# Performance work log

Measured on AMD Instinct MI355X. Metric: run time of the kernel, lower is better.

The kernel has to match this reference:

```python
import jax, jax.numpy as jnp
import numpy as np

NUM_CODES = 1296
D_DIM = 64


def setup_inputs() -> dict:
    key = jax.random.key(0)
    k1, k2 = jax.random.split(key)
    inputs = jax.random.normal(k1, (32, 64, 64, D_DIM), dtype=jnp.float32)
    # lecun_normal init: stddev = 1/sqrt(fan_in) with fan_in = d
    embeddings = jax.random.normal(k2, (NUM_CODES, D_DIM), dtype=jnp.float32) / np.sqrt(D_DIM)
    return {"inputs": inputs, "embeddings": embeddings}


def reference(inputs, embeddings):
    x1 = jnp.sum(inputs ** 2, axis=-1, keepdims=True)          # [b,m,n,1]
    x2 = jnp.sum(embeddings ** 2, axis=-1)                      # [k]
    x3 = jnp.einsum('bmnd,kd->bmnk', inputs, embeddings)        # [b,m,n,k]
    D = x1 + x2 - 2.0 * x3
    codes = jnp.argmin(D, axis=-1).astype(jnp.int32)            # [b,m,n]
    code_vecs = embeddings[codes]                               # [b,m,n,d]
    return codes, code_vecs
```

## Files before the change

### kernel.cpp

```cpp
#include <hip/hip_runtime.h>

#define NUM_CODES 1296
#define PAD_CODES 1344
#define DDIM 64
#define NUM_Q 131072
#define THREADS 256
#define QPW 32
#define QPB 128
#define MARGIN 0.25f
#define CAP 512
#define CHUNK 96
#define NSTEP 14
#define TPC 6

typedef __attribute__((ext_vector_type(8))) short bf16x8;
typedef __attribute__((ext_vector_type(4))) float f32x4;

__device__ __forceinline__ ushort f2bf(float f) {
    unsigned u = __float_as_uint(f);
    return (ushort)((u + 0x7fffu + ((u >> 16) & 1u)) >> 16);
}

__global__ __launch_bounds__(64) void vq_prep(const float* __restrict__ emb,
                                              float* __restrict__ enorm,
                                              ushort* __restrict__ eh) {
    int k = blockIdx.x * 64 + threadIdx.x;
    if (k >= PAD_CODES) return;
    int ks = k < NUM_CODES ? k : NUM_CODES - 1;
    const float* e = emb + (size_t)ks * DDIM;
    float f[DDIM];
#pragma unroll
    for (int i = 0; i < 16; ++i) {
        float4 v = *(const float4*)(e + 4 * i);
        f[4*i] = v.x; f[4*i+1] = v.y; f[4*i+2] = v.z; f[4*i+3] = v.w;
    }
    {
#pragma clang fp contract(off)
        float r8[8];
#pragma unroll
        for (int j = 0; j < 8; ++j) { float t = f[j] * f[j]; r8[j] = t; }
#pragma unroll
        for (int i = 1; i < 8; ++i) {
#pragma unroll
            for (int j = 0; j < 8; ++j) { float t = f[i*8+j] * f[i*8+j]; r8[j] += t; }
        }
        enorm[k] = ((r8[0]+r8[1])+(r8[2]+r8[3])) + ((r8[4]+r8[5])+(r8[6]+r8[7]));
    }
    ushort h[DDIM];
#pragma unroll
    for (int d = 0; d < DDIM; ++d) h[d] = f2bf(f[d]);
    uint* dh = (uint*)(eh + (size_t)k * DDIM);
#pragma unroll
    for (int s = 0; s < 8; ++s) {
        int ds = s ^ (k & 7);
#pragma unroll
        for (int j = 0; j < 4; ++j)
            dh[ds*4 + j] = (uint)h[s*8 + 2*j] | ((uint)h[s*8 + 2*j + 1] << 16);
    }
}

__global__ __launch_bounds__(256) void vq_xnorm(const float* __restrict__ x,
                                                float* __restrict__ xnorm) {
    int q = blockIdx.x * 256 + threadIdx.x;
    const float* r = x + (size_t)q * DDIM;
    float f[DDIM];
#pragma unroll
    for (int i = 0; i < 16; ++i) {
        float4 v = *(const float4*)(r + 4 * i);
        f[4*i] = v.x; f[4*i+1] = v.y; f[4*i+2] = v.z; f[4*i+3] = v.w;
    }
    {
#pragma clang fp contract(off)
        float r8[8];
#pragma unroll
        for (int j = 0; j < 8; ++j) { float t = f[j] * f[j]; r8[j] = t; }
#pragma unroll
        for (int i = 1; i < 8; ++i) {
#pragma unroll
            for (int j = 0; j < 8; ++j) { float t = f[i*8+j] * f[i*8+j]; r8[j] += t; }
        }
        xnorm[q] = ((r8[0]+r8[1])+(r8[2]+r8[3])) + ((r8[4]+r8[5])+(r8[6]+r8[7]));
    }
}

__global__ __launch_bounds__(THREADS) void vq_main(
        const float* __restrict__ x, const float* __restrict__ emb,
        const float* __restrict__ enorm_g, const float* __restrict__ xnorm,
        const ushort* __restrict__ eh, float* __restrict__ out) {
    __shared__ ushort sbuf[2][CHUNK * DDIM];
    __shared__ unsigned wq[4][CAP];
    __shared__ unsigned wcnt[4];
    __shared__ unsigned long long best64[4][QPW];

    const int tid  = threadIdx.x;
    const int lane = tid & 63;
    const int w    = tid >> 6;
    const int cl   = lane & 15;
    const int g    = lane >> 4;
    const long qw  = (long)blockIdx.x * QPB + w * QPW;

    if (lane < QPW) best64[w][lane] = ~0ULL;
    if (lane == 0) wcnt[w] = 0;

    bf16x8 a00, a01, a10, a11;
    {
        const float* xp0 = x + (qw + cl) * DDIM + g * 8;
        const float* xp1 = xp0 + 16 * DDIM;
#pragma unroll
        for (int j = 0; j < 8; ++j) {
            a00[j] = (short)f2bf(xp0[j]);
            a01[j] = (short)f2bf(xp0[j + 32]);
            a10[j] = (short)f2bf(xp1[j]);
            a11[j] = (short)f2bf(xp1[j + 32]);
        }
    }

    float rmin0[4], rmin1[4];
#pragma unroll
    for (int r = 0; r < 4; ++r) { rmin0[r] = __builtin_inff(); rmin1[r] = __builtin_inff(); }

    const int slot0 = (g     ^ (cl & 7)) * 8;
    const int slot1 = ((g+4) ^ (cl & 7)) * 8;

    {
        const float4* src = (const float4*)eh;
        float4 s0 = src[tid], s1 = src[256 + tid], s2 = src[512 + tid];
        *(float4*)&sbuf[0][(size_t)tid * 8]         = s0;
        *(float4*)&sbuf[0][(size_t)(256 + tid) * 8] = s1;
        *(float4*)&sbuf[0][(size_t)(512 + tid) * 8] = s2;
    }
    __syncthreads();
    int cur = 0;
    for (int s = 0; s < NSTEP; ++s) {
        float4 n0, n1, n2;
        const bool more = (s + 1 < NSTEP);
        if (more) {
            const float4* src = (const float4*)(eh + (size_t)(s + 1) * CHUNK * DDIM);
            n0 = src[tid]; n1 = src[256 + tid]; n2 = src[512 + tid];
        }
        const int cb = s * CHUNK;
        float en[TPC];
#pragma unroll
        for (int t = 0; t < TPC; ++t) en[t] = enorm_g[cb + t * 16 + cl];
#pragma unroll
        for (int t = 0; t < TPC; ++t) {
            const ushort* bp = &sbuf[cur][(size_t)(t * 16 + cl) * DDIM];
            bf16x8 b0 = *(const bf16x8*)(bp + slot0);
            bf16x8 b1 = *(const bf16x8*)(bp + slot1);
            f32x4 c00 = {0,0,0,0}, c01 = {0,0,0,0}, c10 = {0,0,0,0}, c11 = {0,0,0,0};
            c00 = __builtin_amdgcn_mfma_f32_16x16x32_bf16(a00, b0, c00, 0, 0, 0);
            c10 = __builtin_amdgcn_mfma_f32_16x16x32_bf16(a10, b0, c10, 0, 0, 0);
            c01 = __builtin_amdgcn_mfma_f32_16x16x32_bf16(a01, b1, c01, 0, 0, 0);
            c11 = __builtin_amdgcn_mfma_f32_16x16x32_bf16(a11, b1, c11, 0, 0, 0);
#pragma unroll
            for (int r = 0; r < 4; ++r) {
                rmin0[r] = fminf(rmin0[r], fmaf(-2.f, c00[r] + c01[r], en[t]));
                rmin1[r] = fminf(rmin1[r], fmaf(-2.f, c10[r] + c11[r], en[t]));
            }
        }
        if (more) {
            *(float4*)&sbuf[cur ^ 1][(size_t)tid * 8]         = n0;
            *(float4*)&sbuf[cur ^ 1][(size_t)(256 + tid) * 8] = n1;
            *(float4*)&sbuf[cur ^ 1][(size_t)(512 + tid) * 8] = n2;
        }
        __syncthreads();
        cur ^= 1;
    }

#pragma unroll
    for (int m = 1; m < 16; m <<= 1) {
#pragma unroll
        for (int r = 0; r < 4; ++r) {
            rmin0[r] = fminf(rmin0[r], __shfl_xor(rmin0[r], m, 64));
            rmin1[r] = fminf(rmin1[r], __shfl_xor(rmin1[r], m, 64));
        }
    }
#pragma unroll
    for (int r = 0; r < 4; ++r) { rmin0[r] += MARGIN; rmin1[r] += MARGIN; }

    {
        const float4* src = (const float4*)eh;
        float4 s0 = src[tid], s1 = src[256 + tid], s2 = src[512 + tid];
        *(float4*)&sbuf[cur][(size_t)tid * 8]         = s0;
        *(float4*)&sbuf[cur][(size_t)(256 + tid) * 8] = s1;
        *(float4*)&sbuf[cur][(size_t)(512 + tid) * 8] = s2;
    }
    __syncthreads();
    for (int s = 0; s < NSTEP; ++s) {
        float4 n0, n1, n2;
        const bool more = (s + 1 < NSTEP);
        if (more) {
            const float4* src = (const float4*)(eh + (size_t)(s + 1) * CHUNK * DDIM);
            n0 = src[tid]; n1 = src[256 + tid]; n2 = src[512 + tid];
        }
        const int cb = s * CHUNK;
        float en[TPC];
#pragma unroll
        for (int t = 0; t < TPC; ++t) en[t] = enorm_g[cb + t * 16 + cl];
#pragma unroll
        for (int t = 0; t < TPC; ++t) {
            const ushort* bp = &sbuf[cur][(size_t)(t * 16 + cl) * DDIM];
            bf16x8 b0 = *(const bf16x8*)(bp + slot0);
            bf16x8 b1 = *(const bf16x8*)(bp + slot1);
            f32x4 c00 = {0,0,0,0}, c01 = {0,0,0,0}, c10 = {0,0,0,0}, c11 = {0,0,0,0};
            c00 = __builtin_amdgcn_mfma_f32_16x16x32_bf16(a00, b0, c00, 0, 0, 0);
            c10 = __builtin_amdgcn_mfma_f32_16x16x32_bf16(a10, b0, c10, 0, 0, 0);
            c01 = __builtin_amdgcn_mfma_f32_16x16x32_bf16(a01, b1, c01, 0, 0, 0);
            c11 = __builtin_amdgcn_mfma_f32_16x16x32_bf16(a11, b1, c11, 0, 0, 0);
            const int c_ = cb + t * 16 + cl;
#pragma unroll
            for (int r = 0; r < 4; ++r) {
                float s0_ = fmaf(-2.f, c00[r] + c01[r], en[t]);
                float s1_ = fmaf(-2.f, c10[r] + c11[r], en[t]);
                if (c_ < NUM_CODES && s0_ <= rmin0[r]) {
                    unsigned i_ = atomicAdd(&wcnt[w], 1u);
                    if (i_ < CAP) wq[w][i_] = ((unsigned)(g*4 + r) << 11) | (unsigned)c_;
                }
                if (c_ < NUM_CODES && s1_ <= rmin1[r]) {
                    unsigned i_ = atomicAdd(&wcnt[w], 1u);
                    if (i_ < CAP) wq[w][i_] = ((unsigned)(16 + g*4 + r) << 11) | (unsigned)c_;
                }
            }
        }
        if (more) {
            *(float4*)&sbuf[cur ^ 1][(size_t)tid * 8]         = n0;
            *(float4*)&sbuf[cur ^ 1][(size_t)(256 + tid) * 8] = n1;
            *(float4*)&sbuf[cur ^ 1][(size_t)(512 + tid) * 8] = n2;
        }
        __syncthreads();
        cur ^= 1;
    }

    unsigned cnt = wcnt[w]; if (cnt > CAP) cnt = CAP;
    for (unsigned i = lane; i < cnt; i += 64) {
        unsigned p = wq[w][i];
        int ql = (int)(p >> 11); int c = (int)(p & 0x7FFu);
        long gq = qw + ql;
        const float* xr = x + gq * DDIM;
        const float* er = emb + (size_t)c * DDIM;
        float dot = 0.f;
#pragma unroll
        for (int p4 = 0; p4 < 16; ++p4) {
            float4 xv = *(const float4*)(xr + 4 * p4);
            float4 ev = *(const float4*)(er + 4 * p4);
            dot = fmaf(xv.x, ev.x, dot); dot = fmaf(xv.y, ev.y, dot);
            dot = fmaf(xv.z, ev.z, dot); dot = fmaf(xv.w, ev.w, dot);
        }
        float dist = (xnorm[gq] + enorm_g[c]) - 2.f * dot;
        unsigned u = __float_as_uint(dist);
        unsigned key = (u & 0x80000000u) ? ~u : (u | 0x80000000u);
        unsigned long long pk = ((unsigned long long)key << 32) | (unsigned)c;
        atomicMin(&best64[w][ql], pk);
    }
    __syncthreads();

#pragma unroll
    for (int qq = 0; qq < 8; ++qq) {
        int ql = qq * 4 + g;
        unsigned kk = (unsigned)(best64[w][ql] & 0xFFFFFFFFu);
        long gq = qw + ql;
        if (cl == 0) out[gq] = (float)kk;
        *(float4*)(out + (long)NUM_Q + gq * DDIM + cl * 4) =
            *(const float4*)(emb + (size_t)kk * DDIM + cl * 4);
    }
}

extern "C" void kernel_launch(void* const* d_in, const int* in_sizes, int n_in,
                              void* d_out, int out_size, void* d_ws, size_t ws_size,
                              hipStream_t stream) {
    const float* x   = (const float*)d_in[0];
    const float* emb = (const float*)d_in[1];
    float*  enorm = (float*)d_ws;
    float*  xnorm = (float*)((char*)d_ws + 8192);
    ushort* eh    = (ushort*)((char*)d_ws + 532480);

    hipLaunchKernelGGL(vq_prep, dim3(PAD_CODES / 64), dim3(64), 0, stream,
                       emb, enorm, eh);
    hipLaunchKernelGGL(vq_xnorm, dim3(NUM_Q / 256), dim3(256), 0, stream,
                       x, xnorm);
    hipLaunchKernelGGL(vq_main, dim3(NUM_Q / QPB), dim3(THREADS), 0, stream,
                       x, emb, enorm, xnorm, eh, (float*)d_out);
}
```

Baseline: 138.9 us.

## Fuse two codebook sweeps into one pass with running-min candidate filter

Drops the separate min-finding sweep over the codebook. A single MFMA pass now keeps a running per-query minimum, seeded by scoring the first chunk twice, and enqueues any code within the margin of the current minimum. Candidates go into per-query slot lists instead of one shared warp queue. A query whose list overflows falls back to an exact scan of the full codebook. This roughly halves the bf16 matmul and shared-memory work, at the cost of more candidates early in the sweep, more LDS atomics, and a possible slow brute-force path for queries that overflow.

```diff
diff --git a/kernel.cpp b/kernel.cpp
--- a/kernel.cpp
+++ b/kernel.cpp
@@ -8,7 +8,7 @@
 #define QPW 32
 #define QPB 128
 #define MARGIN 0.25f
-#define CAP 512
+#define SLOTS 24
 #define CHUNK 96
 #define NSTEP 14
 #define TPC 6
@@ -88,9 +88,9 @@
         const float* __restrict__ enorm_g, const float* __restrict__ xnorm,
         const ushort* __restrict__ eh, float* __restrict__ out) {
     __shared__ ushort sbuf[2][CHUNK * DDIM];
-    __shared__ unsigned wq[4][CAP];
-    __shared__ unsigned wcnt[4];
-    __shared__ unsigned long long best64[4][QPW];
+    __shared__ ushort wq[4][QPW * SLOTS];
+    __shared__ unsigned qcnt[4][QPW];
+    __shared__ unsigned skk[4][QPW];
 
     const int tid  = threadIdx.x;
     const int lane = tid & 63;
@@ -99,8 +99,7 @@
     const int g    = lane >> 4;
     const long qw  = (long)blockIdx.x * QPB + w * QPW;
 
-    if (lane < QPW) best64[w][lane] = ~0ULL;
-    if (lane == 0) wcnt[w] = 0;
+    if (lane < QPW) qcnt[w][lane] = 0;
 
     bf16x8 a00, a01, a10, a11;
     {
@@ -122,77 +121,9 @@
     const int slot0 = (g     ^ (cl & 7)) * 8;
     const int slot1 = ((g+4) ^ (cl & 7)) * 8;
 
-    {
-        const float4* src = (const float4*)eh;
-        float4 s0 = src[tid], s1 = src[256 + tid], s2 = src[512 + tid];
-        *(float4*)&sbuf[0][(size_t)tid * 8]         = s0;
-        *(float4*)&sbuf[0][(size_t)(256 + tid) * 8] = s1;
-        *(float4*)&sbuf[0][(size_t)(512 + tid) * 8] = s2;
-    }
-    __syncthreads();
     int cur = 0;
-    for (int s = 0; s < NSTEP; ++s) {
-        float4 n0, n1, n2;
-        const bool more = (s + 1 < NSTEP);
-        if (more) {
-            const float4* src = (const float4*)(eh + (size_t)(s + 1) * CHUNK * DDIM);
-            n0 = src[tid]; n1 = src[256 + tid]; n2 = src[512 + tid];
-        }
-        const int cb = s * CHUNK;
-        float en[TPC];
-#pragma unroll
-        for (int t = 0; t < TPC; ++t) en[t] = enorm_g[cb + t * 16 + cl];
-#pragma unroll
-        for (int t = 0; t < TPC; ++t) {
-            const ushort* bp = &sbuf[cur][(size_t)(t * 16 + cl) * DDIM];
-            bf16x8 b0 = *(const bf16x8*)(bp + slot0);
-            bf16x8 b1 = *(const bf16x8*)(bp + slot1);
-            f32x4 c00 = {0,0,0,0}, c01 = {0,0,0,0}, c10 = {0,0,0,0}, c11 = {0,0,0,0};
-            c00 = __builtin_amdgcn_mfma_f32_16x16x32_bf16(a00, b0, c00, 0, 0, 0);
-            c10 = __builtin_amdgcn_mfma_f32_16x16x32_bf16(a10, b0, c10, 0, 0, 0);
-            c01 = __builtin_amdgcn_mfma_f32_16x16x32_bf16(a01, b1, c01, 0, 0, 0);
-            c11 = __builtin_amdgcn_mfma_f32_16x16x32_bf16(a11, b1, c11, 0, 0, 0);
-#pragma unroll
-            for (int r = 0; r < 4; ++r) {
-                rmin0[r] = fminf(rmin0[r], fmaf(-2.f, c00[r] + c01[r], en[t]));
-                rmin1[r] = fminf(rmin1[r], fmaf(-2.f, c10[r] + c11[r], en[t]));
-            }
-        }
-        if (more) {
-            *(float4*)&sbuf[cur ^ 1][(size_t)tid * 8]         = n0;
-            *(float4*)&sbuf[cur ^ 1][(size_t)(256 + tid) * 8] = n1;
-            *(float4*)&sbuf[cur ^ 1][(size_t)(512 + tid) * 8] = n2;
-        }
-        __syncthreads();
-        cur ^= 1;
-    }
-
-#pragma unroll
-    for (int m = 1; m < 16; m <<= 1) {
-#pragma unroll
-        for (int r = 0; r < 4; ++r) {
-            rmin0[r] = fminf(rmin0[r], __shfl_xor(rmin0[r], m, 64));
-            rmin1[r] = fminf(rmin1[r], __shfl_xor(rmin1[r], m, 64));
-        }
-    }
-#pragma unroll
-    for (int r = 0; r < 4; ++r) { rmin0[r] += MARGIN; rmin1[r] += MARGIN; }
-
-    {
-        const float4* src = (const float4*)eh;
-        float4 s0 = src[tid], s1 = src[256 + tid], s2 = src[512 + tid];
-        *(float4*)&sbuf[cur][(size_t)tid * 8]         = s0;
-        *(float4*)&sbuf[cur][(size_t)(256 + tid) * 8] = s1;
-        *(float4*)&sbuf[cur][(size_t)(512 + tid) * 8] = s2;
-    }
-    __syncthreads();
-    for (int s = 0; s < NSTEP; ++s) {
-        float4 n0, n1, n2;
-        const bool more = (s + 1 < NSTEP);
-        if (more) {
-            const float4* src = (const float4*)(eh + (size_t)(s + 1) * CHUNK * DDIM);
-            n0 = src[tid]; n1 = src[256 + tid]; n2 = src[512 + tid];
-        }
+
+    auto pass = [&](int s, bool do_enq) {
         const int cb = s * CHUNK;
         float en[TPC];
 #pragma unroll
@@ -212,16 +143,56 @@
             for (int r = 0; r < 4; ++r) {
                 float s0_ = fmaf(-2.f, c00[r] + c01[r], en[t]);
                 float s1_ = fmaf(-2.f, c10[r] + c11[r], en[t]);
-                if (c_ < NUM_CODES && s0_ <= rmin0[r]) {
-                    unsigned i_ = atomicAdd(&wcnt[w], 1u);
-                    if (i_ < CAP) wq[w][i_] = ((unsigned)(g*4 + r) << 11) | (unsigned)c_;
+                rmin0[r] = fminf(rmin0[r], s0_);
+                rmin1[r] = fminf(rmin1[r], s1_);
+                if (do_enq && c_ < NUM_CODES) {
+                    if (s0_ <= rmin0[r] + MARGIN) {
+                        unsigned i_ = atomicAdd(&qcnt[w][g*4 + r], 1u);
+                        if (i_ < SLOTS) wq[w][(g*4 + r) * SLOTS + i_] = (ushort)c_;
+                    }
+                    if (s1_ <= rmin1[r] + MARGIN) {
+                        unsigned i_ = atomicAdd(&qcnt[w][16 + g*4 + r], 1u);
+                        if (i_ < SLOTS) wq[w][(16 + g*4 + r) * SLOTS + i_] = (ushort)c_;
+                    }
                 }
-                if (c_ < NUM_CODES && s1_ <= rmin1[r]) {
-                    unsigned i_ = atomicAdd(&wcnt[w], 1u);
-                    if (i_ < CAP) wq[w][i_] = ((unsigned)(16 + g*4 + r) << 11) | (unsigned)c_;
-                }
-            }
-        }
+            }
+        }
+    };
+    auto reduce_rmin = [&]() {
+#pragma unroll
+        for (int m = 1; m < 16; m <<= 1) {
+#pragma unroll
+            for (int r = 0; r < 4; ++r) {
+                rmin0[r] = fminf(rmin0[r], __shfl_xor(rmin0[r], m, 64));
+                rmin1[r] = fminf(rmin1[r], __shfl_xor(rmin1[r], m, 64));
+            }
+        }
+    };
+
+    {
+        const float4* src = (const float4*)eh;
+        float4 s0 = src[tid], s1 = src[256 + tid], s2 = src[512 + tid];
+        *(float4*)&sbuf[0][(size_t)tid * 8]         = s0;
+        *(float4*)&sbuf[0][(size_t)(256 + tid) * 8] = s1;
+        *(float4*)&sbuf[0][(size_t)(512 + tid) * 8] = s2;
+    }
+    __syncthreads();
+
+    for (int s = 0; s < NSTEP; ++s) {
+        float4 n0, n1, n2;
+        const bool more = (s + 1 < NSTEP);
+        if (more) {
+            const float4* src = (const float4*)(eh + (size_t)(s + 1) * CHUNK * DDIM);
+            n0 = src[tid]; n1 = src[256 + tid]; n2 = src[512 + tid];
+        }
+        if (s == 0) {
+            pass(0, false);
+            reduce_rmin();
+            pass(0, true);
+        } else {
+            pass(s, true);
+        }
+        reduce_rmin();
         if (more) {
             *(float4*)&sbuf[cur ^ 1][(size_t)tid * 8]         = n0;
             *(float4*)&sbuf[cur ^ 1][(size_t)(256 + tid) * 8] = n1;
@@ -231,11 +202,7 @@
         cur ^= 1;
     }
 
-    unsigned cnt = wcnt[w]; if (cnt > CAP) cnt = CAP;
-    for (unsigned i = lane; i < cnt; i += 64) {
-        unsigned p = wq[w][i];
-        int ql = (int)(p >> 11); int c = (int)(p & 0x7FFu);
-        long gq = qw + ql;
+    auto exact_pk = [&](int c, long gq) -> unsigned long long {
         const float* xr = x + gq * DDIM;
         const float* er = emb + (size_t)c * DDIM;
         float dot = 0.f;
@@ -249,19 +216,62 @@
         float dist = (xnorm[gq] + enorm_g[c]) - 2.f * dot;
         unsigned u = __float_as_uint(dist);
         unsigned key = (u & 0x80000000u) ? ~u : (u | 0x80000000u);
-        unsigned long long pk = ((unsigned long long)key << 32) | (unsigned)c;
-        atomicMin(&best64[w][ql], pk);
-    }
-    __syncthreads();
-
-#pragma unroll
-    for (int qq = 0; qq < 8; ++qq) {
-        int ql = qq * 4 + g;
-        unsigned kk = (unsigned)(best64[w][ql] & 0xFFFFFFFFu);
-        long gq = qw + ql;
-        if (cl == 0) out[gq] = (float)kk;
-        *(float4*)(out + (long)NUM_Q + gq * DDIM + cl * 4) =
-            *(const float4*)(emb + (size_t)kk * DDIM + cl * 4);
+        return ((unsigned long long)key << 32) | (unsigned)c;
+    };
+
+    const int grp = lane >> 3, gl = lane & 7;
+#pragma unroll
+    for (int qo = 0; qo < 4; ++qo) {
+        const int ql = qo * 8 + grp;
+        const long gq = qw + ql;
+        const unsigned nq = qcnt[w][ql];
+        unsigned long long pk = ~0ULL;
+        if (nq <= SLOTS) {
+            for (unsigned i = gl; i < nq; i += 8) {
+                unsigned long long t = exact_pk((int)wq[w][ql * SLOTS + i], gq);
+                if (t < pk) pk = t;
+            }
+        }
+#pragma unroll
+        for (int m = 1; m < 8; m <<= 1) {
+            unsigned long long o = (unsigned long long)__shfl_xor((long long)pk, m, 64);
+            if (o < pk) pk = o;
+        }
+        if (gl == 0 && nq <= SLOTS) {
+            skk[w][ql] = (unsigned)pk;
+            out[gq] = (float)(unsigned)pk;
+        }
+    }
+    for (int ql = 0; ql < QPW; ++ql) {
+        if (qcnt[w][ql] <= SLOTS) continue;
+        const long gq = qw + ql;
+        unsigned long long pk = ~0ULL;
+        for (int t = 0; t < 21; ++t) {
+            int c = lane + (t << 6);
+            if (c < NUM_CODES) {
+                unsigned long long tp = exact_pk(c, gq);
+                if (tp < pk) pk = tp;
+            }
+        }
+#pragma unroll
+        for (int m = 1; m < 64; m <<= 1) {
+            unsigned long long o = (unsigned long long)__shfl_xor((long long)pk, m, 64);
+            if (o < pk) pk = o;
+        }
+        if (lane == 0) {
+            skk[w][ql] = (unsigned)pk;
+            out[gq] = (float)(unsigned)pk;
+        }
+    }
+
+    const int gu = lane >> 4, gv = lane & 15;
+#pragma unroll
+    for (int qo = 0; qo < 8; ++qo) {
+        const int ql = qo * 4 + gu;
+        const unsigned kk = skk[w][ql];
+        const long gq = qw + ql;
+        *(float4*)(out + (long)NUM_Q + gq * DDIM + gv * 4) =
+            *(const float4*)(emb + (size_t)kk * DDIM + gv * 4);
     }
 }
 
```

Measured after the change: 175.5 us. 26.3% more time.
